# Kernel optimization log

Hardware: AMD Instinct MI355X
Metric: run time of the kernel (lower is better)

Reference implementation:

```python
import jax, jax.numpy as jnp
import numpy as np
import math

G_GRAPHS = 32   # graphs per batch
NPG = 2048      # nodes per graph
DEG = 8         # avg degree
IN_DIM = 128
HID = 128

def _lin(k, fi, fo):
    return jax.random.normal(k, (fi, fo), jnp.float32) / np.sqrt(fi).astype(np.float32)

def setup_inputs():
    key = jax.random.key(0)
    ks = jax.random.split(key, 32)
    Nt = G_GRAPHS * NPG
    Epg = NPG * DEG
    E = G_GRAPHS * Epg
    x = jax.random.normal(ks[0], (Nt, IN_DIM), jnp.float32)
    src = jax.random.randint(ks[1], (E,), 0, NPG)
    dst = jax.random.randint(ks[2], (E,), 0, NPG)
    off = (jnp.arange(E) // Epg) * NPG  # keep edges within their graph block
    edge_index = jnp.stack([src + off, dst + off]).astype(jnp.int32)
    batch = (jnp.arange(Nt) // NPG).astype(jnp.int32)
    p = {}
    dims = [(IN_DIM, HID), (HID, HID), (HID, HID), (HID, HID)]
    for i, (fi, fo) in enumerate(dims, 1):
        p['Wl%d' % i] = _lin(ks[3 * i], fi, fo)
        p['bl%d' % i] = jnp.zeros((fo,), jnp.float32)
        p['Wr%d' % i] = _lin(ks[3 * i + 1], fi, fo)
    for j in (1, 2):  # SAGPooling score GNN (GraphConv hidden->1)
        p['Prel%d' % j] = _lin(ks[15 + 2 * j], HID, 1)
        p['prb%d' % j] = jnp.zeros((1,), jnp.float32)
        p['Proot%d' % j] = _lin(ks[16 + 2 * j], HID, 1)
    p['W5'] = _lin(ks[24], HID, 64); p['b5'] = jnp.zeros((64,), jnp.float32)
    p['W6'] = _lin(ks[25], 64, 2);  p['b6'] = jnp.zeros((2,), jnp.float32)
    return dict(x=x, edge_index=edge_index, batch=batch, npg=NPG, **p)

def reference(x, edge_index, batch, npg,
              Wl1, bl1, Wr1, Wl2, bl2, Wr2, Wl3, bl3, Wr3, Wl4, bl4, Wr4,
              Prel1, prb1, Proot1, Prel2, prb2, Proot2, W5, b5, W6, b6):
    src, dst = edge_index[0], edge_index[1]
    Nt = x.shape[0]
    Gn = Nt // npg

    def sage(h, em, Wl, bl, Wr):
        # SAGEConv (mean aggr): lin_l(mean_j x_j) + lin_r(x_root)
        s = jax.ops.segment_sum(h[src] * em[:, None], dst, num_segments=Nt)
        c = jax.ops.segment_sum(em, dst, num_segments=Nt)
        return (s / jnp.maximum(c, 1.0)[:, None]) @ Wl + bl + h @ Wr

    def pool(h, em, nm, k, Prel, prb, Proot):
        # SAGPooling: score = GraphConv(h) (add aggr), top-k per graph, x *= tanh(score)
        s = jax.ops.segment_sum(h[src] * em[:, None], dst, num_segments=Nt)
        score = (s @ Prel + h @ Proot + prb)[:, 0]
        smr = jnp.where(nm > 0, score, -1e30).reshape(Gn, npg)
        _, idx = jax.lax.top_k(smr, k)
        newm = jnp.zeros((Gn, npg), h.dtype).at[jnp.arange(Gn)[:, None], idx].set(1.0).reshape(-1)
        h = h * jnp.tanh(score)[:, None] * newm[:, None]
        em = em * newm[src] * newm[dst]  # filter_adj: keep edges with both ends kept
        return h, em, newm

    em = jnp.ones(src.shape, x.dtype)
    nm = jnp.ones((Nt,), x.dtype)
    h = jax.nn.relu(sage(x, em, Wl1, bl1, Wr1))
    h = jax.nn.relu(sage(h, em, Wl2, bl2, Wr2))
    k1 = math.ceil(0.5 * npg)
    h, em, nm = pool(h, em, nm, k1, Prel1, prb1, Proot1)
    h = jax.nn.relu(sage(h, em, Wl3, bl3, Wr3)) * nm[:, None]
    h = jax.nn.relu(sage(h, em, Wl4, bl4, Wr4)) * nm[:, None]
    k2 = math.ceil(0.5 * k1)
    h, em, nm = pool(h, em, nm, k2, Prel2, prb2, Proot2)
    # global mean pool over surviving nodes
    sums = jax.ops.segment_sum(h, batch, num_segments=Gn)
    cnt = jax.ops.segment_sum(nm, batch, num_segments=Gn)
    g = sums / jnp.maximum(cnt, 1.0)[:, None]
    g = jax.nn.relu(g @ W5 + b5)
    return jax.nn.log_softmax(g @ W6 + b6, axis=1)
```

## Files before the change

### kernel.cpp

```cpp
#include <hip/hip_runtime.h>
#include <hip/hip_bf16.h>
#include <math.h>

#define NT   65536
#define NPGC 2048
#define NG   32
#define NE   524288
#define HID  128

typedef short short8 __attribute__((ext_vector_type(8)));
typedef float f32x4  __attribute__((ext_vector_type(4)));

__device__ __forceinline__ float bf2f(unsigned short u) {
    union { unsigned int i; float f; } v; v.i = ((unsigned int)u) << 16; return v.f;
}
__device__ __forceinline__ unsigned short f2bf(float f) {
    union { float f; unsigned int i; } v; v.f = f;
    unsigned int x = v.i;
    return (unsigned short)((x + 0x7fffu + ((x >> 16) & 1u)) >> 16);
}

__global__ void k_detect(const unsigned short* __restrict__ x, int* __restrict__ flag) {
    __shared__ int cnt;
    if (threadIdx.x == 0) cnt = 0;
    __syncthreads();
    int sane = 0;
#pragma unroll
    for (int j = 0; j < 16; ++j) {
        unsigned short u = x[threadIdx.x * 16 + j];
        int e = (u >> 7) & 0xFF;
        if (e > 0x60 && e < 0xA0) sane++;
    }
    atomicAdd(&cnt, sane);
    __syncthreads();
    if (threadIdx.x == 0) *flag = (cnt > 3686) ? 1 : 0;
}

struct CvtDesc { const void* src[22]; int n[22]; int off[22]; };

__global__ void k_cvt(CvtDesc d, float* __restrict__ wts, const int* __restrict__ flag) {
    int t = blockIdx.y;
    int n = d.n[t];
    bool isbf = (*flag != 0);
    const unsigned short* sb = (const unsigned short*)d.src[t];
    const float* sf = (const float*)d.src[t];
    float* o = wts + d.off[t];
    for (int i = blockIdx.x * blockDim.x + threadIdx.x; i < n; i += gridDim.x * blockDim.x)
        o[i] = isbf ? bf2f(sb[i]) : sf[i];
}

__global__ void k_packW(const float* __restrict__ wts, int4 oWl, int4 oWr,
                        unsigned short* __restrict__ Wpack,
                        int* __restrict__ rowc, int* __restrict__ fill) {
    int idx = blockIdx.x * 256 + threadIdx.x;
    if (idx < NT) { rowc[idx] = 0; fill[idx] = 0; }
    if (idx >= 4 * 8 * 8 * 64 * 8) return;
    int L    = idx >> 15;
    int rem  = idx & 32767;
    int ct   = rem >> 12;
    int rem2 = rem & 4095;
    int ks   = rem2 >> 9;
    int rem3 = rem2 & 511;
    int lane = rem3 >> 3;
    int j    = rem3 & 7;
    int k   = ks * 32 + (lane >> 4) * 8 + j;
    int col = ct * 16 + (lane & 15);
    int ol = (L == 0) ? oWl.x : (L == 1) ? oWl.y : (L == 2) ? oWl.z : oWl.w;
    int orr = (L == 0) ? oWr.x : (L == 1) ? oWr.y : (L == 2) ? oWr.z : oWr.w;
    float w = (k < 128) ? wts[ol + k * 128 + col] : wts[orr + (k - 128) * 128 + col];
    unsigned short hi = f2bf(w);
    unsigned short lo = f2bf(w - bf2f(hi));
    int base = L * 65536 + (ct * 8 + ks) * 512 + lane * 8 + j;
    Wpack[base]         = hi;
    Wpack[base + 32768] = lo;
}

__global__ void k_load_x(const void* __restrict__ x, float* __restrict__ out,
                         const int* __restrict__ flag, int n4,
                         float* __restrict__ nm, const int* __restrict__ dstE,
                         int* __restrict__ rowc) {
    int i = blockIdx.x * blockDim.x + threadIdx.x;
    if (i < NT) nm[i] = 1.0f;
    if (i < NE) atomicAdd(&rowc[dstE[i]], 1);
    if (i >= n4) return;
    if (*flag) {
        ushort4 v = ((const ushort4*)x)[i];
        float4 o;
        o.x = bf2f(v.x); o.y = bf2f(v.y); o.z = bf2f(v.z); o.w = bf2f(v.w);
        ((float4*)out)[i] = o;
    } else {
        ((float4*)out)[i] = ((const float4*)x)[i];
    }
}

__global__ void k_scan1(const int* __restrict__ cnt, int* __restrict__ rp, int* __restrict__ bsum,
                        float* __restrict__ invc) {
    __shared__ int s[256];
    int t = threadIdx.x;
    int i = blockIdx.x * 256 + t;
    int v = cnt[i];
    invc[i] = 1.0f / fmaxf((float)v, 1.0f);
    s[t] = v;
    __syncthreads();
    for (int off = 1; off < 256; off <<= 1) {
        int a = (t >= off) ? s[t - off] : 0;
        __syncthreads();
        s[t] += a;
        __syncthreads();
    }
    rp[i] = s[t] - v;
    if (t == 255) bsum[blockIdx.x] = s[255];
}

__global__ void k_scan2(const int* __restrict__ bsum, int* __restrict__ boff) {
    __shared__ int s[256];
    int t = threadIdx.x;
    int v = bsum[t];
    s[t] = v;
    __syncthreads();
    for (int off = 1; off < 256; off <<= 1) {
        int a = (t >= off) ? s[t - off] : 0;
        __syncthreads();
        s[t] += a;
        __syncthreads();
    }
    boff[t] = s[t] - v;
}

__global__ void k_scan3(int* __restrict__ rp, const int* __restrict__ boff) {
    int i = blockIdx.x * 256 + threadIdx.x;
    rp[i] += boff[i >> 8];
    if (i == 0) rp[NT] = NE;
}

__global__ void k_scatter(const int* __restrict__ src, const int* __restrict__ dst,
                          const int* __restrict__ rp, int* __restrict__ fill, int* __restrict__ col) {
    int e = blockIdx.x * blockDim.x + threadIdx.x;
    if (e < NE) {
        int d = dst[e];
        int p = rp[d] + atomicAdd(&fill[d], 1);
        col[p] = src[e];
    }
}

__global__ void k_invc(const float* __restrict__ nm, const int* __restrict__ rp,
                       const int* __restrict__ col, float* __restrict__ invc) {
    int n = blockIdx.x * 256 + threadIdx.x;
    int beg = rp[n], end = rp[n + 1];
    float c = 0.f;
    for (int e = beg; e < end; ++e) c += nm[col[e]];
    invc[n] = 1.0f / fmaxf(c, 1.0f);
}

__device__ __forceinline__ int lds_sw(int node, int k) {
    int g = k >> 3;
    int go = g ^ (node & 7);
    return node * 128 + go * 8 + (k & 7);
}

template<bool HAS_TS>
__device__ __forceinline__ void sage_body(
    const float* __restrict__ h, const float* __restrict__ ts,
    const float* __restrict__ nm, const float* __restrict__ invc,
    const int* __restrict__ rp, const int* __restrict__ col,
    const unsigned short* __restrict__ Wp,
    unsigned short* Ahi, unsigned short* Alo,
    int n0, int tid, f32x4 acc[2][2])
{
    int lane = tid & 63, w = tid >> 6;
    int lrow = lane & 15, quad = lane >> 4;

#pragma unroll
    for (int pass = 0; pass < 4; ++pass) {
        int node = pass * 8 + (tid >> 5);
        int f = (tid & 31) * 4;
        int gn = n0 + node;
        float ax = 0.f, ay = 0.f, az = 0.f, aw = 0.f;
        if (nm[gn] > 0.f) {
            int beg = rp[gn], end = rp[gn + 1];
            for (int e0 = beg; e0 < end; e0 += 4) {
                int ecl = end - 1;
                int e1 = (e0 + 1 < end) ? e0 + 1 : ecl;
                int e2 = (e0 + 2 < end) ? e0 + 2 : ecl;
                int e3 = (e0 + 3 < end) ? e0 + 3 : ecl;
                int s0 = col[e0], s1 = col[e1], s2 = col[e2], s3 = col[e3];
                float4 v0 = *(const float4*)&h[(size_t)s0 * HID + f];
                float4 v1 = *(const float4*)&h[(size_t)s1 * HID + f];
                float4 v2 = *(const float4*)&h[(size_t)s2 * HID + f];
                float4 v3 = *(const float4*)&h[(size_t)s3 * HID + f];
                float c0 = HAS_TS ? ts[s0] : 1.0f;
                float c1 = (e0 + 1 < end) ? (HAS_TS ? ts[s1] : 1.0f) : 0.0f;
                float c2 = (e0 + 2 < end) ? (HAS_TS ? ts[s2] : 1.0f) : 0.0f;
                float c3 = (e0 + 3 < end) ? (HAS_TS ? ts[s3] : 1.0f) : 0.0f;
                ax += v0.x * c0 + v1.x * c1 + v2.x * c2 + v3.x * c3;
                ay += v0.y * c0 + v1.y * c1 + v2.y * c2 + v3.y * c3;
                az += v0.z * c0 + v1.z * c1 + v2.z * c2 + v3.z * c3;
                aw += v0.w * c0 + v1.w * c1 + v2.w * c2 + v3.w * c3;
            }
        }
        float inv = invc[gn];
        float m0 = ax * inv, m1 = ay * inv, m2 = az * inv, m3 = aw * inv;
        ushort4 hi4, lo4;
        hi4.x = f2bf(m0); lo4.x = f2bf(m0 - bf2f(hi4.x));
        hi4.y = f2bf(m1); lo4.y = f2bf(m1 - bf2f(hi4.y));
        hi4.z = f2bf(m2); lo4.z = f2bf(m2 - bf2f(hi4.z));
        hi4.w = f2bf(m3); lo4.w = f2bf(m3 - bf2f(hi4.w));
        int a = lds_sw(node, f);
        *(ushort4*)&Ahi[a] = hi4;
        *(ushort4*)&Alo[a] = lo4;
    }
    __syncthreads();

#pragma unroll
    for (int ks = 0; ks < 4; ++ks) {
        short8 bh[2], blo[2];
#pragma unroll
        for (int c = 0; c < 2; ++c) {
            int ct = 2 * w + c;
            bh[c]  = *(const short8*)&Wp[(ct * 8 + ks) * 512 + lane * 8];
            blo[c] = *(const short8*)&Wp[32768 + (ct * 8 + ks) * 512 + lane * 8];
        }
        int kb = ks * 32 + quad * 8;
#pragma unroll
        for (int st = 0; st < 2; ++st) {
            int a = lds_sw(st * 16 + lrow, kb);
            short8 ah = *(const short8*)&Ahi[a];
            short8 al = *(const short8*)&Alo[a];
#pragma unroll
            for (int c = 0; c < 2; ++c) {
                acc[st][c] = __builtin_amdgcn_mfma_f32_16x16x32_bf16(ah, bh[c],  acc[st][c], 0, 0, 0);
                acc[st][c] = __builtin_amdgcn_mfma_f32_16x16x32_bf16(al, bh[c],  acc[st][c], 0, 0, 0);
                acc[st][c] = __builtin_amdgcn_mfma_f32_16x16x32_bf16(ah, blo[c], acc[st][c], 0, 0, 0);
            }
        }
    }
    __syncthreads();

#pragma unroll
    for (int i = 0; i < 4; ++i) {
        int idx = i * 256 + tid;
        int node = idx >> 5;
        int f = (idx & 31) * 4;
        int gn = n0 + node;
        float4 v = *(const float4*)&h[(size_t)gn * HID + f];
        float sc = HAS_TS ? ts[gn] : 1.0f;
        float v0 = v.x * sc, v1 = v.y * sc, v2 = v.z * sc, v3 = v.w * sc;
        ushort4 hi4, lo4;
        hi4.x = f2bf(v0); lo4.x = f2bf(v0 - bf2f(hi4.x));
        hi4.y = f2bf(v1); lo4.y = f2bf(v1 - bf2f(hi4.y));
        hi4.z = f2bf(v2); lo4.z = f2bf(v2 - bf2f(hi4.z));
        hi4.w = f2bf(v3); lo4.w = f2bf(v3 - bf2f(hi4.w));
        int a = lds_sw(node, f);
        *(ushort4*)&Ahi[a] = hi4;
        *(ushort4*)&Alo[a] = lo4;
    }
    __syncthreads();

#pragma unroll
    for (int ks = 4; ks < 8; ++ks) {
        short8 bh[2], blo[2];
#pragma unroll
        for (int c = 0; c < 2; ++c) {
            int ct = 2 * w + c;
            bh[c]  = *(const short8*)&Wp[(ct * 8 + ks) * 512 + lane * 8];
            blo[c] = *(const short8*)&Wp[32768 + (ct * 8 + ks) * 512 + lane * 8];
        }
        int kb = (ks - 4) * 32 + quad * 8;
#pragma unroll
        for (int st = 0; st < 2; ++st) {
            int a = lds_sw(st * 16 + lrow, kb);
            short8 ah = *(const short8*)&Ahi[a];
            short8 al = *(const short8*)&Alo[a];
#pragma unroll
            for (int c = 0; c < 2; ++c) {
                acc[st][c] = __builtin_amdgcn_mfma_f32_16x16x32_bf16(ah, bh[c],  acc[st][c], 0, 0, 0);
                acc[st][c] = __builtin_amdgcn_mfma_f32_16x16x32_bf16(al, bh[c],  acc[st][c], 0, 0, 0);
                acc[st][c] = __builtin_amdgcn_mfma_f32_16x16x32_bf16(ah, blo[c], acc[st][c], 0, 0, 0);
            }
        }
    }
}

template<bool HAS_TS>
__global__ void __launch_bounds__(256, 8) k_sage_plain(
    const float* __restrict__ h, const float* __restrict__ ts,
    const float* __restrict__ nm, const float* __restrict__ invc,
    const int* __restrict__ rp, const int* __restrict__ col,
    const unsigned short* __restrict__ Wp, const float* __restrict__ bl,
    float* __restrict__ out)
{
    __shared__ unsigned short Ahi[32 * 128];
    __shared__ unsigned short Alo[32 * 128];
    int tid = threadIdx.x;
    int b = blockIdx.x;
    int graph = (b & 7) * 4 + (b >> 9);
    int tile  = (b >> 3) & 63;
    int n0 = graph * NPGC + tile * 32;
    int lane = tid & 63, w = tid >> 6;
    int lrow = lane & 15, quad = lane >> 4;
    f32x4 acc[2][2] = {};

    sage_body<HAS_TS>(h, ts, nm, invc, rp, col, Wp, Ahi, Alo, n0, tid, acc);

#pragma unroll
    for (int c = 0; c < 2; ++c) {
        int colg = (2 * w + c) * 16 + lrow;
        float bias = bl[colg];
#pragma unroll
        for (int st = 0; st < 2; ++st) {
#pragma unroll
            for (int rr = 0; rr < 4; ++rr) {
                int node = n0 + st * 16 + quad * 4 + rr;
                float val = fmaxf(acc[st][c][rr] + bias, 0.f) * nm[node];
                out[(size_t)node * HID + colg] = val;
            }
        }
    }
}

__global__ void __launch_bounds__(256, 8) k_sage_dots(
    const float* __restrict__ h,
    const float* __restrict__ nm, const float* __restrict__ invc,
    const int* __restrict__ rp, const int* __restrict__ col,
    const unsigned short* __restrict__ Wp, const float* __restrict__ bl,
    float* __restrict__ out,
    const float* __restrict__ Prel, const float* __restrict__ Proot,
    float* __restrict__ q, float* __restrict__ r)
{
    __shared__ unsigned short Ahi[32 * 128];
    __shared__ unsigned short Alo[32 * 128];
    int tid = threadIdx.x;
    int b = blockIdx.x;
    int graph = (b & 7) * 4 + (b >> 9);
    int tile  = (b >> 3) & 63;
    int n0 = graph * NPGC + tile * 32;
    int lane = tid & 63, w = tid >> 6;
    int lrow = lane & 15, quad = lane >> 4;
    f32x4 acc[2][2] = {};

    sage_body<false>(h, nullptr, nm, invc, rp, col, Wp, Ahi, Alo, n0, tid, acc);

    float qp[2][4] = {}, rp_[2][4] = {};
#pragma unroll
    for (int c = 0; c < 2; ++c) {
        int colg = (2 * w + c) * 16 + lrow;
        float bias = bl[colg];
        float pq = Prel[colg], pr = Proot[colg];
#pragma unroll
        for (int st = 0; st < 2; ++st) {
#pragma unroll
            for (int rr = 0; rr < 4; ++rr) {
                int node = n0 + st * 16 + quad * 4 + rr;
                float val = fmaxf(acc[st][c][rr] + bias, 0.f) * nm[node];
                out[(size_t)node * HID + colg] = val;
                qp[st][rr] += val * pq;
                rp_[st][rr] += val * pr;
            }
        }
    }
#pragma unroll
    for (int st = 0; st < 2; ++st)
#pragma unroll
        for (int rr = 0; rr < 4; ++rr) {
#pragma unroll
            for (int m = 1; m < 16; m <<= 1) {
                qp[st][rr]  += __shfl_xor(qp[st][rr],  m, 64);
                rp_[st][rr] += __shfl_xor(rp_[st][rr], m, 64);
            }
        }
    __syncthreads();
    float* qa = (float*)Ahi;
    if (tid < 64) qa[tid] = 0.f;
    __syncthreads();
    if (lrow == 0) {
#pragma unroll
        for (int st = 0; st < 2; ++st)
#pragma unroll
            for (int rr = 0; rr < 4; ++rr) {
                int nl = st * 16 + quad * 4 + rr;
                atomicAdd(&qa[nl], qp[st][rr]);
                atomicAdd(&qa[32 + nl], rp_[st][rr]);
            }
    }
    __syncthreads();
    if (tid < 32) {
        q[n0 + tid] = qa[tid];
        r[n0 + tid] = qa[32 + tid];
    }
}

__global__ void k_score(const float* __restrict__ q, const float* __restrict__ r,
                        const float* __restrict__ prb,
                        const int* __restrict__ rp, const int* __restrict__ col,
                        float* __restrict__ score) {
    int n = blockIdx.x * 256 + threadIdx.x;
    int beg = rp[n], end = rp[n + 1];
    float s = 0.f;
    for (int e = beg; e < end; ++e) s += q[col[e]];
    score[n] = s + r[n] + prb[0];
}

__global__ void __launch_bounds__(256) k_topk(const float* __restrict__ score,
                                              float* __restrict__ nm,
                                              float* __restrict__ tval, int k) {
    __shared__ unsigned int u[NPGC];
    __shared__ int hist[256];
    __shared__ int scanb[256];
    __shared__ unsigned int s_byte;
    __shared__ int s_kk;
    int tid = threadIdx.x;
    int base = blockIdx.x * NPGC;

    for (int j = tid; j < NPGC; j += 256) {
        float sc = (nm[base + j] > 0.f) ? score[base + j] : -1e30f;
        unsigned int v = __float_as_uint(sc);
        v = (v & 0x80000000u) ? ~v : (v | 0x80000000u);
        u[j] = v;
    }
    __syncthreads();

    unsigned int prefix = 0;
    int kk = k;
#pragma unroll
    for (int round = 0; round < 4; ++round) {
        int shift = 24 - 8 * round;
        unsigned int pmask = (round == 0) ? 0u : (0xFFFFFFFFu << (32 - 8 * round));
        hist[tid] = 0;
        __syncthreads();
        for (int j = tid; j < NPGC; j += 256) {
            unsigned int v = u[j];
            if ((v & pmask) == prefix) atomicAdd(&hist[(v >> shift) & 0xFF], 1);
        }
        __syncthreads();
        scanb[tid] = hist[tid];
        __syncthreads();
        for (int off = 1; off < 256; off <<= 1) {
            int add = (tid + off < 256) ? scanb[tid + off] : 0;
            __syncthreads();
            scanb[tid] += add;
            __syncthreads();
        }
        int above = (tid == 255) ? 0 : scanb[tid + 1];
        if (scanb[tid] >= kk && above < kk) {
            s_byte = (unsigned int)tid;
            s_kk = kk - above;
        }
        __syncthreads();
        prefix |= (s_byte << shift);
        kk = s_kk;
        __syncthreads();
    }
    unsigned int thr = prefix;
    int j0 = tid * 8;
    int cnt = 0;
#pragma unroll
    for (int j = 0; j < 8; ++j) cnt += (u[j0 + j] == thr);
    scanb[tid] = cnt;
    __syncthreads();
    for (int off = 1; off < 256; off <<= 1) {
        int add = (tid >= off) ? scanb[tid - off] : 0;
        __syncthreads();
        scanb[tid] += add;
        __syncthreads();
    }
    int rank = scanb[tid] - cnt;
#pragma unroll
    for (int j = 0; j < 8; ++j) {
        unsigned int v = u[j0 + j];
        bool keep;
        if (v > thr) keep = true;
        else if (v == thr) { keep = (rank < kk); rank++; }
        else keep = false;
        nm[base + j0 + j]   = keep ? 1.0f : 0.0f;
        tval[base + j0 + j] = keep ? tanhf(score[base + j0 + j]) : 0.0f;
    }
}

__global__ void k_gsum(const float* __restrict__ h, const float* __restrict__ t,
                       const float* __restrict__ nm,
                       float* __restrict__ g, float* __restrict__ gcnt) {
    int b = blockIdx.x;
    int graph = b >> 4, part = b & 15;
    int f = threadIdx.x & 127, sub = threadIdx.x >> 7;
    int nbase = graph * NPGC + part * 128 + sub * 64;
    float acc = 0.f;
#pragma unroll 4
    for (int n = 0; n < 64; ++n)
        acc += h[(size_t)(nbase + n) * HID + f] * t[nbase + n];
    atomicAdd(&g[graph * HID + f], acc);
    if (threadIdx.x < 64 && sub == 0) {
        float cnt = 0.f;
        int cb = graph * NPGC + part * 128;
        for (int n = threadIdx.x; n < 128; n += 64) cnt += nm[cb + n];
        for (int o = 32; o > 0; o >>= 1) cnt += __shfl_down(cnt, o, 64);
        if (threadIdx.x == 0) atomicAdd(&gcnt[graph], cnt);
    }
}

__global__ void k_mlp(const float* __restrict__ g, const float* __restrict__ gcnt,
                      const float* __restrict__ W5,
                      const float* __restrict__ b5, const float* __restrict__ W6,
                      const float* __restrict__ b6, void* __restrict__ out,
                      const int* __restrict__ flag) {
    __shared__ float g5[64];
    __shared__ float ls[2];
    int graph = blockIdx.x, j = threadIdx.x;
    float ic = 1.0f / fmaxf(gcnt[graph], 1.0f);
    float acc = b5[j];
    for (int f = 0; f < HID; ++f)
        acc += (g[graph * HID + f] * ic) * W5[f * 64 + j];
    g5[j] = fmaxf(acc, 0.f);
    __syncthreads();
    if (j < 2) {
        float l = b6[j];
        for (int t = 0; t < 64; ++t) l += g5[t] * W6[t * 2 + j];
        ls[j] = l;
    }
    __syncthreads();
    if (j == 0) {
        float a = ls[0], b = ls[1];
        float mx = fmaxf(a, b);
        float lse = mx + logf(expf(a - mx) + expf(b - mx));
        if (*flag) {
            ((unsigned short*)out)[graph * 2 + 0] = f2bf(a - lse);
            ((unsigned short*)out)[graph * 2 + 1] = f2bf(b - lse);
        } else {
            ((float*)out)[graph * 2 + 0] = a - lse;
            ((float*)out)[graph * 2 + 1] = b - lse;
        }
    }
}

extern "C" void kernel_launch(void* const* d_in, const int* in_sizes, int n_in,
                              void* d_out, int out_size, void* d_ws, size_t ws_size,
                              hipStream_t stream) {
    const void* x    = d_in[0];
    const int*  ei   = (const int*)d_in[1];
    const int*  srcE = ei;
    const int*  dstE = ei + NE;

    char* ws = (char*)d_ws;
    float* hA    = (float*)(ws + 0);
    float* hB    = (float*)(ws + 33554432);
    float* tvec  = (float*)(ws + 67108864);
    float* invc  = (float*)(ws + 67371008);
    float* q     = (float*)(ws + 100663296);
    float* r     = (float*)(ws + 100925440);
    float* score = (float*)(ws + 101187584);
    float* nm    = (float*)(ws + 101449728);
    int*   rowc  = (int*)  (ws + 101711872);
    int*   rp    = (int*)  (ws + 101974016);
    int*   bsum  = (int*)  (ws + 102236416);
    int*   boff  = (int*)  (ws + 102237440);
    int*   fill  = (int*)  (ws + 102238464);
    int*   col   = (int*)  (ws + 102500608);
    float* g     = (float*)(ws + 104597760);
    float* gcnt  = (float*)(ws + 104614144);
    int*   flag  = (int*)  (ws + 104615936);
    float* wts   = (float*)(ws + 104616960);
    unsigned short* Wpack = (unsigned short*)(ws + 105179136);
    (void)in_sizes; (void)n_in; (void)out_size; (void)ws_size;

    const int O_Wl1 = 0,      O_bl1 = 16384,  O_Wr1 = 16512;
    const int O_Wl2 = 32896,  O_bl2 = 49280,  O_Wr2 = 49408;
    const int O_Wl3 = 65792,  O_bl3 = 82176,  O_Wr3 = 82304;
    const int O_Wl4 = 98688,  O_bl4 = 115072, O_Wr4 = 115200;
    const int O_Pr1 = 131584, O_pb1 = 131712, O_Po1 = 131713;
    const int O_Pr2 = 131841, O_pb2 = 131969, O_Po2 = 131970;
    const int O_W5  = 132098, O_b5  = 140290, O_W6 = 140354, O_b6 = 140482;

    CvtDesc d;
    const int srcIdx[22] = {4,5,6,7,8,9,10,11,12,13,14,15,16,17,18,19,20,21,22,23,24,25};
    const int nelems[22] = {16384,128,16384, 16384,128,16384, 16384,128,16384, 16384,128,16384,
                            128,1,128, 128,1,128, 8192,64,128,2};
    const int offs[22]   = {O_Wl1,O_bl1,O_Wr1, O_Wl2,O_bl2,O_Wr2, O_Wl3,O_bl3,O_Wr3, O_Wl4,O_bl4,O_Wr4,
                            O_Pr1,O_pb1,O_Po1, O_Pr2,O_pb2,O_Po2, O_W5,O_b5,O_W6,O_b6};
    for (int i = 0; i < 22; ++i) { d.src[i] = d_in[srcIdx[i]]; d.n[i] = nelems[i]; d.off[i] = offs[i]; }

    hipMemsetAsync(g, 0, (NG * HID + NG + 64) * 4, stream);

    k_detect <<<1, 256, 0, stream>>>((const unsigned short*)x, flag);
    k_cvt    <<<dim3(64, 22), 256, 0, stream>>>(d, wts, flag);
    k_packW  <<<512, 256, 0, stream>>>(wts, make_int4(O_Wl1, O_Wl2, O_Wl3, O_Wl4),
                                       make_int4(O_Wr1, O_Wr2, O_Wr3, O_Wr4), Wpack, rowc, fill);
    k_load_x <<<8192, 256, 0, stream>>>(x, hA, flag, NT * HID / 4, nm, dstE, rowc);

    k_scan1  <<<256, 256, 0, stream>>>(rowc, rp, bsum, invc);
    k_scan2  <<<1, 256, 0, stream>>>(bsum, boff);
    k_scan3  <<<256, 256, 0, stream>>>(rp, boff);
    k_scatter<<<2048, 256, 0, stream>>>(srcE, dstE, rp, fill, col);

    k_sage_plain<false><<<2048, 256, 0, stream>>>(hA, nullptr, nm, invc, rp, col,
                                                  Wpack + 0 * 65536, wts + O_bl1, hB);
    k_sage_dots<<<2048, 256, 0, stream>>>(hB, nm, invc, rp, col,
                                          Wpack + 1 * 65536, wts + O_bl2, hA,
                                          wts + O_Pr1, wts + O_Po1, q, r);

    k_score<<<256, 256, 0, stream>>>(q, r, wts + O_pb1, rp, col, score);
    k_topk <<<32, 256, 0, stream>>>(score, nm, tvec, 1024);
    k_invc <<<256, 256, 0, stream>>>(nm, rp, col, invc);

    k_sage_plain<true><<<2048, 256, 0, stream>>>(hA, tvec, nm, invc, rp, col,
                                                 Wpack + 2 * 65536, wts + O_bl3, hB);
    k_sage_dots<<<2048, 256, 0, stream>>>(hB, nm, invc, rp, col,
                                          Wpack + 3 * 65536, wts + O_bl4, hA,
                                          wts + O_Pr2, wts + O_Po2, q, r);

    k_score<<<256, 256, 0, stream>>>(q, r, wts + O_pb2, rp, col, score);
    k_topk <<<32, 256, 0, stream>>>(score, nm, tvec, 512);

    k_gsum<<<512, 256, 0, stream>>>(hA, tvec, nm, g, gcnt);
    k_mlp <<<32, 64, 0, stream>>>(g, gcnt, wts + O_W5, wts + O_b5, wts + O_W6, wts + O_b6, d_out, flag);
}
```

Measured before the change: 392.8 us.

## Read fp32 input directly in first SAGE layer, merge scan kernels, cheaper bf16 split

When the input is already fp32, the first SAGE layer now reads x directly instead of first copying it into a workspace buffer, which removes a 32 MB copy pass. The second and third prefix-scan kernels are merged: every block redoes the small 256-element scan itself, saving one launch. The hi/lo bf16 split now truncates instead of rounding to nearest, which cuts ALU work in the LDS staging loops. Truncating the hi part gives a slightly different error split, though hi+lo still approximates the value closely.

```diff
diff --git a/kernel.cpp b/kernel.cpp
--- a/kernel.cpp
+++ b/kernel.cpp
@@ -18,6 +18,12 @@
     union { float f; unsigned int i; } v; v.f = f;
     unsigned int x = v.i;
     return (unsigned short)((x + 0x7fffu + ((x >> 16) & 1u)) >> 16);
+}
+__device__ __forceinline__ void split2(float v, unsigned short& hi, unsigned short& lo) {
+    unsigned int b = __float_as_uint(v);
+    hi = (unsigned short)(b >> 16);
+    float rem = v - __uint_as_float(b & 0xFFFF0000u);
+    lo = (unsigned short)(__float_as_uint(rem) >> 16);
 }
 
 __global__ void k_detect(const unsigned short* __restrict__ x, int* __restrict__ flag) {
@@ -88,8 +94,6 @@
         float4 o;
         o.x = bf2f(v.x); o.y = bf2f(v.y); o.z = bf2f(v.z); o.w = bf2f(v.w);
         ((float4*)out)[i] = o;
-    } else {
-        ((float4*)out)[i] = ((const float4*)x)[i];
     }
 }
 
@@ -112,11 +116,10 @@
     if (t == 255) bsum[blockIdx.x] = s[255];
 }
 
-__global__ void k_scan2(const int* __restrict__ bsum, int* __restrict__ boff) {
+__global__ void k_scan23(int* __restrict__ rp, const int* __restrict__ bsum) {
     __shared__ int s[256];
     int t = threadIdx.x;
-    int v = bsum[t];
-    s[t] = v;
+    s[t] = bsum[t];
     __syncthreads();
     for (int off = 1; off < 256; off <<= 1) {
         int a = (t >= off) ? s[t - off] : 0;
@@ -124,12 +127,9 @@
         s[t] += a;
         __syncthreads();
     }
-    boff[t] = s[t] - v;
-}
-
-__global__ void k_scan3(int* __restrict__ rp, const int* __restrict__ boff) {
-    int i = blockIdx.x * 256 + threadIdx.x;
-    rp[i] += boff[i >> 8];
+    int boffv = s[blockIdx.x] - bsum[blockIdx.x];
+    int i = blockIdx.x * 256 + t;
+    rp[i] += boffv;
     if (i == 0) rp[NT] = NE;
 }
 
@@ -199,12 +199,11 @@
             }
         }
         float inv = invc[gn];
-        float m0 = ax * inv, m1 = ay * inv, m2 = az * inv, m3 = aw * inv;
         ushort4 hi4, lo4;
-        hi4.x = f2bf(m0); lo4.x = f2bf(m0 - bf2f(hi4.x));
-        hi4.y = f2bf(m1); lo4.y = f2bf(m1 - bf2f(hi4.y));
-        hi4.z = f2bf(m2); lo4.z = f2bf(m2 - bf2f(hi4.z));
-        hi4.w = f2bf(m3); lo4.w = f2bf(m3 - bf2f(hi4.w));
+        split2(ax * inv, hi4.x, lo4.x);
+        split2(ay * inv, hi4.y, lo4.y);
+        split2(az * inv, hi4.z, lo4.z);
+        split2(aw * inv, hi4.w, lo4.w);
         int a = lds_sw(node, f);
         *(ushort4*)&Ahi[a] = hi4;
         *(ushort4*)&Alo[a] = lo4;
@@ -244,12 +243,11 @@
         int gn = n0 + node;
         float4 v = *(const float4*)&h[(size_t)gn * HID + f];
         float sc = HAS_TS ? ts[gn] : 1.0f;
-        float v0 = v.x * sc, v1 = v.y * sc, v2 = v.z * sc, v3 = v.w * sc;
         ushort4 hi4, lo4;
-        hi4.x = f2bf(v0); lo4.x = f2bf(v0 - bf2f(hi4.x));
-        hi4.y = f2bf(v1); lo4.y = f2bf(v1 - bf2f(hi4.y));
-        hi4.z = f2bf(v2); lo4.z = f2bf(v2 - bf2f(hi4.z));
-        hi4.w = f2bf(v3); lo4.w = f2bf(v3 - bf2f(hi4.w));
+        split2(v.x * sc, hi4.x, lo4.x);
+        split2(v.y * sc, hi4.y, lo4.y);
+        split2(v.z * sc, hi4.z, lo4.z);
+        split2(v.w * sc, hi4.w, lo4.w);
         int a = lds_sw(node, f);
         *(ushort4*)&Ahi[a] = hi4;
         *(ushort4*)&Alo[a] = lo4;
@@ -283,7 +281,8 @@
 
 template<bool HAS_TS>
 __global__ void __launch_bounds__(256, 8) k_sage_plain(
-    const float* __restrict__ h, const float* __restrict__ ts,
+    const float* __restrict__ h, const void* __restrict__ xraw, const int* __restrict__ flag,
+    const float* __restrict__ ts,
     const float* __restrict__ nm, const float* __restrict__ invc,
     const int* __restrict__ rp, const int* __restrict__ col,
     const unsigned short* __restrict__ Wp, const float* __restrict__ bl,
@@ -300,7 +299,10 @@
     int lrow = lane & 15, quad = lane >> 4;
     f32x4 acc[2][2] = {};
 
-    sage_body<HAS_TS>(h, ts, nm, invc, rp, col, Wp, Ahi, Alo, n0, tid, acc);
+    const float* hh = h;
+    if (xraw && *flag == 0) hh = (const float*)xraw;
+
+    sage_body<HAS_TS>(hh, ts, nm, invc, rp, col, Wp, Ahi, Alo, n0, tid, acc);
 
 #pragma unroll
     for (int c = 0; c < 2; ++c) {
@@ -551,7 +553,6 @@
     int*   rowc  = (int*)  (ws + 101711872);
     int*   rp    = (int*)  (ws + 101974016);
     int*   bsum  = (int*)  (ws + 102236416);
-    int*   boff  = (int*)  (ws + 102237440);
     int*   fill  = (int*)  (ws + 102238464);
     int*   col   = (int*)  (ws + 102500608);
     float* g     = (float*)(ws + 104597760);
@@ -586,11 +587,10 @@
     k_load_x <<<8192, 256, 0, stream>>>(x, hA, flag, NT * HID / 4, nm, dstE, rowc);
 
     k_scan1  <<<256, 256, 0, stream>>>(rowc, rp, bsum, invc);
-    k_scan2  <<<1, 256, 0, stream>>>(bsum, boff);
-    k_scan3  <<<256, 256, 0, stream>>>(rp, boff);
+    k_scan23 <<<256, 256, 0, stream>>>(rp, bsum);
     k_scatter<<<2048, 256, 0, stream>>>(srcE, dstE, rp, fill, col);
 
-    k_sage_plain<false><<<2048, 256, 0, stream>>>(hA, nullptr, nm, invc, rp, col,
+    k_sage_plain<false><<<2048, 256, 0, stream>>>(hA, x, flag, nullptr, nm, invc, rp, col,
                                                   Wpack + 0 * 65536, wts + O_bl1, hB);
     k_sage_dots<<<2048, 256, 0, stream>>>(hB, nm, invc, rp, col,
                                           Wpack + 1 * 65536, wts + O_bl2, hA,
@@ -600,7 +600,7 @@
     k_topk <<<32, 256, 0, stream>>>(score, nm, tvec, 1024);
     k_invc <<<256, 256, 0, stream>>>(nm, rp, col, invc);
 
-    k_sage_plain<true><<<2048, 256, 0, stream>>>(hA, tvec, nm, invc, rp, col,
+    k_sage_plain<true><<<2048, 256, 0, stream>>>(hA, nullptr, flag, tvec, nm, invc, rp, col,
                                                  Wpack + 2 * 65536, wts + O_bl3, hB);
     k_sage_dots<<<2048, 256, 0, stream>>>(hB, nm, invc, rp, col,
                                           Wpack + 3 * 65536, wts + O_bl4, hA,
```

New measurement: 391.0 us. No clear change (-0.5%).
